# Optimization experiments

Hardware: AMD Instinct MI355X
Metric: run time of the kernel (lower is better)

The kernel has to match this reference:

```python
import jax, jax.numpy as jnp
import numpy as np


def setup_inputs() -> dict:
    key = jax.random.key(0)
    k1, k2 = jax.random.split(key)
    B, Tq, Tk, D = 8, 2048, 2048, 1024
    decoder_hidden = jax.random.normal(k1, (B, Tq, D), dtype=jnp.float32)
    encoder_outputs = jax.random.normal(k2, (B, Tk, D), dtype=jnp.float32)
    return {"decoder_hidden": decoder_hidden, "encoder_outputs": encoder_outputs}


def reference(decoder_hidden, encoder_outputs):
    # scores: [B, Tq, Tk] = decoder_hidden @ encoder_outputs^T (no scaling, as in source)
    scores = jnp.einsum("bqd,bkd->bqk", decoder_hidden, encoder_outputs)
    attention_weights = jax.nn.softmax(scores, axis=2)
    # context: [B, Tq, D]
    context_vector = jnp.einsum("bqk,bkd->bqd", attention_weights, encoder_outputs)
    return (context_vector, attention_weights)
```

## Files before the change

### kernel.cpp

```cpp
#include <hip/hip_runtime.h>


typedef _Float16 f16;
typedef _Float16 half4 __attribute__((ext_vector_type(4)));
typedef _Float16 half8 __attribute__((ext_vector_type(8)));
typedef float floatx4 __attribute__((ext_vector_type(4)));

#define BM 128
#define BN 128
#define BK 32

__device__ __forceinline__ void gl2lds16(const void* g, void* l) {
    __builtin_amdgcn_global_load_lds(
        (const __attribute__((address_space(1))) unsigned int*)g,
        (__attribute__((address_space(3))) unsigned int*)l,
        16, 0, 0);
}

__global__ __launch_bounds__(256) void cvt_f32_f16(const float* __restrict__ src,
                                                   f16* __restrict__ dst, int n4) {
    int i = blockIdx.x * 256 + threadIdx.x;
    if (i >= n4) return;
    float4 v = ((const float4*)src)[i];
    half4 h;
    h[0] = (f16)v.x; h[1] = (f16)v.y; h[2] = (f16)v.z; h[3] = (f16)v.w;
    ((half4*)dst)[i] = h;
}

__global__ __launch_bounds__(256) void k_cvt_transpose(const float* __restrict__ K,
                                                       f16* __restrict__ Kh,
                                                       f16* __restrict__ Kt) {
    __shared__ f16 tile[32][33];
    const int b  = blockIdx.z;
    const int k0 = blockIdx.y * 32;
    const int d0 = blockIdx.x * 32;
    const int tx = threadIdx.x;
    const int ty = threadIdx.y;
    const float* src = K + (size_t)b * 2048 * 1024;
    f16* khb = Kh + (size_t)b * 2048 * 1024;
    f16* ktb = Kt + (size_t)b * 1024 * 2048;
    #pragma unroll
    for (int i = ty; i < 32; i += 8) {
        f16 v = (f16)src[(size_t)(k0 + i) * 1024 + d0 + tx];
        tile[i][tx] = v;
        khb[(size_t)(k0 + i) * 1024 + d0 + tx] = v;
    }
    __syncthreads();
    #pragma unroll
    for (int i = ty; i < 32; i += 8) {
        ktb[(size_t)(d0 + i) * 2048 + k0 + tx] = tile[tx][i];
    }
}

__global__ __launch_bounds__(256) void gemm_bt(const f16* __restrict__ Amat,
                                               const f16* __restrict__ Bmat,
                                               float* __restrict__ C,
                                               int K_, int N, int nN,
                                               long sA, long sB, long sC) {
    __shared__ f16 As[BM * BK];
    __shared__ f16 Bs[BN * BK];
    const int tid  = threadIdx.x;
    const int lane = tid & 63;
    const int wave = tid >> 6;
    const int wm = (wave & 1) * 64;
    const int wn = (wave >> 1) * 64;
    const int bz = blockIdx.x;
    const int tileM = (blockIdx.y / nN) * BM;
    const int tileN = (blockIdx.y % nN) * BN;
    const f16* Ab = Amat + (size_t)bz * sA;
    const f16* Bb = Bmat + (size_t)bz * sB;
    float* Cb = C + (size_t)bz * sC;

    floatx4 zero = {0.f, 0.f, 0.f, 0.f};
    floatx4 acc[4][4];
    #pragma unroll
    for (int i = 0; i < 4; i++)
        #pragma unroll
        for (int j = 0; j < 4; j++) acc[i][j] = zero;

    for (int k0 = 0; k0 < K_; k0 += BK) {
        #pragma unroll
        for (int r = 0; r < 2; r++) {
            int h = (r * 256 + tid) * 8;
            int row = h >> 5, col = h & 31;
            gl2lds16(Ab + (size_t)(tileM + row) * K_ + k0 + col, &As[h]);
        }
        #pragma unroll
        for (int r = 0; r < 2; r++) {
            int h = (r * 256 + tid) * 8;
            int row = h >> 5, col = h & 31;
            gl2lds16(Bb + (size_t)(tileN + row) * K_ + k0 + col, &Bs[h]);
        }
        __syncthreads();

        const int mr = lane & 15;
        const int kq = (lane >> 4) * 8;
        half8 af[4], bf[4];
        #pragma unroll
        for (int i = 0; i < 4; i++)
            af[i] = *(const half8*)&As[(wm + i * 16 + mr) * BK + kq];
        #pragma unroll
        for (int j = 0; j < 4; j++)
            bf[j] = *(const half8*)&Bs[(wn + j * 16 + mr) * BK + kq];
        #pragma unroll
        for (int i = 0; i < 4; i++)
            #pragma unroll
            for (int j = 0; j < 4; j++)
                acc[i][j] = __builtin_amdgcn_mfma_f32_16x16x32_f16(af[i], bf[j], acc[i][j], 0, 0, 0);
        __syncthreads();
    }

    const int r0 = (lane >> 4) * 4;
    const int cn = lane & 15;
    #pragma unroll
    for (int i = 0; i < 4; i++) {
        #pragma unroll
        for (int j = 0; j < 4; j++) {
            int col = tileN + wn + j * 16 + cn;
            #pragma unroll
            for (int r = 0; r < 4; r++) {
                int row = tileM + wm + i * 16 + r0 + r;
                Cb[(size_t)row * N + col] = acc[i][j][r];
            }
        }
    }
}

__global__ __launch_bounds__(256) void softmax_rows(float* __restrict__ S,
                                                    f16* __restrict__ Wh) {
    const size_t row = blockIdx.x;
    float* p = S + row * 2048;
    f16* ph = Wh + row * 2048;
    const int tid = threadIdx.x;
    const int lane = tid & 63;
    const int wave = tid >> 6;
    __shared__ float red[8];

    float4 va = ((const float4*)p)[tid];
    float4 vb = ((const float4*)p)[tid + 256];
    float m = fmaxf(fmaxf(fmaxf(va.x, va.y), fmaxf(va.z, va.w)),
                    fmaxf(fmaxf(vb.x, vb.y), fmaxf(vb.z, vb.w)));
    #pragma unroll
    for (int off = 32; off; off >>= 1) m = fmaxf(m, __shfl_xor(m, off));
    if (lane == 0) red[wave] = m;
    __syncthreads();
    m = fmaxf(fmaxf(red[0], red[1]), fmaxf(red[2], red[3]));

    va.x = __expf(va.x - m); va.y = __expf(va.y - m);
    va.z = __expf(va.z - m); va.w = __expf(va.w - m);
    vb.x = __expf(vb.x - m); vb.y = __expf(vb.y - m);
    vb.z = __expf(vb.z - m); vb.w = __expf(vb.w - m);
    float s = va.x + va.y + va.z + va.w + vb.x + vb.y + vb.z + vb.w;
    #pragma unroll
    for (int off = 32; off; off >>= 1) s += __shfl_xor(s, off);
    if (lane == 0) red[4 + wave] = s;
    __syncthreads();
    s = red[4] + red[5] + red[6] + red[7];
    float inv = 1.0f / s;
    va.x *= inv; va.y *= inv; va.z *= inv; va.w *= inv;
    vb.x *= inv; vb.y *= inv; vb.z *= inv; vb.w *= inv;
    ((float4*)p)[tid] = va;
    ((float4*)p)[tid + 256] = vb;
    half4 ha, hb;
    ha[0] = (f16)va.x; ha[1] = (f16)va.y; ha[2] = (f16)va.z; ha[3] = (f16)va.w;
    hb[0] = (f16)vb.x; hb[1] = (f16)vb.y; hb[2] = (f16)vb.z; hb[3] = (f16)vb.w;
    ((half4*)ph)[tid] = ha;
    ((half4*)ph)[tid + 256] = hb;
}

extern "C" void kernel_launch(void* const* d_in, const int* in_sizes, int n_in,
                              void* d_out, int out_size, void* d_ws, size_t ws_size,
                              hipStream_t stream) {
    const float* Q = (const float*)d_in[0];
    const float* K = (const float*)d_in[1];
    float* ctx = (float*)d_out;
    float* W   = (float*)d_out + 16777216;

    f16* Qh = (f16*)d_ws;
    f16* Kh = Qh + 16777216;
    f16* Kt = Kh + 16777216;
    f16* Wh = (f16*)d_ws;

    cvt_f32_f16<<<16384, 256, 0, stream>>>(Q, Qh, 4194304);
    k_cvt_transpose<<<dim3(32, 64, 8), dim3(32, 8), 0, stream>>>(K, Kh, Kt);

    gemm_bt<<<dim3(8, 256), 256, 0, stream>>>(
        Qh, Kh, W, 1024, 2048, 16, 2048L * 1024, 2048L * 1024, 2048L * 2048);

    softmax_rows<<<16384, 256, 0, stream>>>(W, Wh);

    gemm_bt<<<dim3(8, 128), 256, 0, stream>>>(
        Wh, Kt, ctx, 2048, 1024, 8, 2048L * 2048, 1024L * 2048, 2048L * 1024);
}
```

Before: 564.1 us.

## Double GEMM K-tile with XOR-swizzled LDS and vectorize K convert-transpose

Raises the GEMM K-tile from 32 to 64 so each barrier pair covers twice as many MFMAs, halving the number of synchronizations per tile. LDS rows are stored with an XOR swizzle on 16-byte chunks to avoid bank conflicts on the wider rows. The K convert/transpose kernel now processes 64x64 tiles with float4 loads and half4 stores. The cost is double the LDS per block, which may lower occupancy.

```diff
diff --git a/kernel.cpp b/kernel.cpp
--- a/kernel.cpp
+++ b/kernel.cpp
@@ -8,7 +8,7 @@
 
 #define BM 128
 #define BN 128
-#define BK 32
+#define BK 64
 
 __device__ __forceinline__ void gl2lds16(const void* g, void* l) {
     __builtin_amdgcn_global_load_lds(
@@ -30,25 +30,32 @@
 __global__ __launch_bounds__(256) void k_cvt_transpose(const float* __restrict__ K,
                                                        f16* __restrict__ Kh,
                                                        f16* __restrict__ Kt) {
-    __shared__ f16 tile[32][33];
+    __shared__ f16 tile[64][72];
     const int b  = blockIdx.z;
-    const int k0 = blockIdx.y * 32;
-    const int d0 = blockIdx.x * 32;
-    const int tx = threadIdx.x;
-    const int ty = threadIdx.y;
+    const int k0 = blockIdx.y * 64;
+    const int d0 = blockIdx.x * 64;
     const float* src = K + (size_t)b * 2048 * 1024;
     f16* khb = Kh + (size_t)b * 2048 * 1024;
     f16* ktb = Kt + (size_t)b * 1024 * 2048;
-    #pragma unroll
-    for (int i = ty; i < 32; i += 8) {
-        f16 v = (f16)src[(size_t)(k0 + i) * 1024 + d0 + tx];
-        tile[i][tx] = v;
-        khb[(size_t)(k0 + i) * 1024 + d0 + tx] = v;
+    const int r  = threadIdx.x >> 4;
+    const int c4 = (threadIdx.x & 15) * 4;
+    #pragma unroll
+    for (int it = 0; it < 4; it++) {
+        int kr = it * 16 + r;
+        float4 v = *(const float4*)&src[(size_t)(k0 + kr) * 1024 + d0 + c4];
+        half4 h;
+        h[0] = (f16)v.x; h[1] = (f16)v.y; h[2] = (f16)v.z; h[3] = (f16)v.w;
+        *(half4*)&khb[(size_t)(k0 + kr) * 1024 + d0 + c4] = h;
+        *(half4*)&tile[kr][c4] = h;
     }
     __syncthreads();
     #pragma unroll
-    for (int i = ty; i < 32; i += 8) {
-        ktb[(size_t)(d0 + i) * 2048 + k0 + tx] = tile[tx][i];
+    for (int it = 0; it < 4; it++) {
+        int dr = it * 16 + r;
+        half4 h;
+        h[0] = tile[c4 + 0][dr]; h[1] = tile[c4 + 1][dr];
+        h[2] = tile[c4 + 2][dr]; h[3] = tile[c4 + 3][dr];
+        *(half4*)&ktb[(size_t)(d0 + dr) * 2048 + k0 + c4] = h;
     }
 }
 
@@ -78,40 +85,48 @@
         #pragma unroll
         for (int j = 0; j < 4; j++) acc[i][j] = zero;
 
+    const int mr = lane & 15;
+    const int q  = lane >> 4;
+    const int sw = mr & 7;
+
     for (int k0 = 0; k0 < K_; k0 += BK) {
         #pragma unroll
-        for (int r = 0; r < 2; r++) {
-            int h = (r * 256 + tid) * 8;
-            int row = h >> 5, col = h & 31;
-            gl2lds16(Ab + (size_t)(tileM + row) * K_ + k0 + col, &As[h]);
-        }
-        #pragma unroll
-        for (int r = 0; r < 2; r++) {
-            int h = (r * 256 + tid) * 8;
-            int row = h >> 5, col = h & 31;
-            gl2lds16(Bb + (size_t)(tileN + row) * K_ + k0 + col, &Bs[h]);
+        for (int r = 0; r < 4; r++) {
+            int h = r * 256 + tid;
+            int row = h >> 3, cc = h & 7;
+            int gcc = cc ^ (row & 7);
+            gl2lds16(Ab + (size_t)(tileM + row) * K_ + k0 + gcc * 8, &As[h * 8]);
+        }
+        #pragma unroll
+        for (int r = 0; r < 4; r++) {
+            int h = r * 256 + tid;
+            int row = h >> 3, cc = h & 7;
+            int gcc = cc ^ (row & 7);
+            gl2lds16(Bb + (size_t)(tileN + row) * K_ + k0 + gcc * 8, &Bs[h * 8]);
         }
         __syncthreads();
 
-        const int mr = lane & 15;
-        const int kq = (lane >> 4) * 8;
-        half8 af[4], bf[4];
-        #pragma unroll
-        for (int i = 0; i < 4; i++)
-            af[i] = *(const half8*)&As[(wm + i * 16 + mr) * BK + kq];
-        #pragma unroll
-        for (int j = 0; j < 4; j++)
-            bf[j] = *(const half8*)&Bs[(wn + j * 16 + mr) * BK + kq];
-        #pragma unroll
-        for (int i = 0; i < 4; i++)
+        #pragma unroll
+        for (int s = 0; s < 2; s++) {
+            const int lc = ((s << 2) | q) ^ sw;
+            half8 af[4], bf[4];
+            #pragma unroll
+            for (int i = 0; i < 4; i++)
+                af[i] = *(const half8*)&As[(wm + i * 16 + mr) * BK + lc * 8];
             #pragma unroll
             for (int j = 0; j < 4; j++)
-                acc[i][j] = __builtin_amdgcn_mfma_f32_16x16x32_f16(af[i], bf[j], acc[i][j], 0, 0, 0);
+                bf[j] = *(const half8*)&Bs[(wn + j * 16 + mr) * BK + lc * 8];
+            #pragma unroll
+            for (int i = 0; i < 4; i++)
+                #pragma unroll
+                for (int j = 0; j < 4; j++)
+                    acc[i][j] = __builtin_amdgcn_mfma_f32_16x16x32_f16(af[i], bf[j], acc[i][j], 0, 0, 0);
+        }
         __syncthreads();
     }
 
-    const int r0 = (lane >> 4) * 4;
-    const int cn = lane & 15;
+    const int r0 = q * 4;
+    const int cn = mr;
     #pragma unroll
     for (int i = 0; i < 4; i++) {
         #pragma unroll
@@ -182,7 +197,7 @@
     f16* Wh = (f16*)d_ws;
 
     cvt_f32_f16<<<16384, 256, 0, stream>>>(Q, Qh, 4194304);
-    k_cvt_transpose<<<dim3(32, 64, 8), dim3(32, 8), 0, stream>>>(K, Kh, Kt);
+    k_cvt_transpose<<<dim3(16, 32, 8), 256, 0, stream>>>(K, Kh, Kt);
 
     gemm_bt<<<dim3(8, 256), 256, 0, stream>>>(
         Qh, Kh, W, 1024, 2048, 16, 2048L * 1024, 2048L * 1024, 2048L * 2048);
```

Result: faster. 524.2 us (-7.1%).
